# Performance work log

Hardware: AMD Instinct MI355X
Metric: run time of the kernel (lower is better)

The kernel has to match this reference:

```python
import jax, jax.numpy as jnp
import numpy as np

N_STEPS = 8          # spatial_interval
SPATIAL_SCALE = 1.0  # spatial_scale


def setup_inputs() -> dict:
    key = jax.random.key(0)
    ks = jax.random.split(key, 6)
    B, N, D = 32, 1024, 256
    x = jax.random.normal(ks[0], (B, N, D), dtype=jnp.float32)
    adj_mx = jax.random.uniform(ks[1], (N, N), dtype=jnp.float32) / N  # row-scaled dense adjacency
    alpha_train = jnp.ones((N,), dtype=jnp.float32)          # alpha * ones(num_node), alpha=1.0
    w = jnp.eye(D, dtype=jnp.float32) + 0.01 * jax.random.normal(ks[2], (D, D), dtype=jnp.float32)
    d = jax.random.uniform(ks[3], (D,), dtype=jnp.float32)
    fc_in_w = jax.random.normal(ks[4], (D, D), dtype=jnp.float32) * (1.0 / np.sqrt(D))
    fc_in_b = jnp.zeros((D,), dtype=jnp.float32)
    return {"x": x, "adj_mx": adj_mx, "alpha_train": alpha_train, "w": w,
            "d": d, "fc_in_w": fc_in_w, "fc_in_b": fc_in_b, "vt": 0}


def reference(x, adj_mx, alpha_train, w, d, fc_in_w, fc_in_b, vt):
    # x: [B, N, D]. x0 is detached in torch (x.clone().detach()).
    x0 = jax.lax.stop_gradient(x)
    # fc_in (dropout is identity in eval mode)
    h = jnp.einsum('bnd,ed->bne', x, fc_in_w) + fc_in_b
    # constants of the diffusion ODE
    alph = jax.nn.sigmoid(alpha_train)[:, None]          # [N, 1]
    d_clamped = jnp.clip(d, 0.0, 1.0)
    w_eff = (w * d_clamped) @ w.T                        # [D, D]
    dt = jnp.float32(SPATIAL_SCALE / N_STEPS)

    def euler_step(h, _):
        ax = jnp.einsum('nm,bmd->bnd', adj_mx, h)        # graph diffusion
        f = alph * 0.5 * (ax - h) + h @ w_eff - h + x0
        return h + dt * f, None

    h, _ = jax.lax.scan(euler_step, h, None, length=N_STEPS)
    return h
```

## Files before the change

### kernel.cpp

```cpp
#include <hip/hip_runtime.h>
#include <hip/hip_bf16.h>
#include <stdint.h>

typedef __bf16 bf16;
typedef __bf16 bf16x8 __attribute__((ext_vector_type(8)));
typedef __bf16 bf16x4 __attribute__((ext_vector_type(4)));
typedef float f32x4 __attribute__((ext_vector_type(4)));
typedef unsigned short u16;

__device__ __forceinline__ void gload_lds16(const bf16* g, bf16* l) {
    __builtin_amdgcn_global_load_lds(
        (const __attribute__((address_space(1))) void*)g,
        (__attribute__((address_space(3))) void*)l, 16, 0, 0);
}

__device__ __forceinline__ void stChunk(const bf16* __restrict__ g, int ld,
                                        bf16* l, int c) {
    int row = c >> 3, slot = c & 7;
    gload_lds16(g + (size_t)row * ld + ((slot ^ (row & 7)) << 3), l + c * 8);
}

__device__ __forceinline__ void mma8(const bf16x8& a0, const bf16x8& a1,
                                     const bf16x8& b0, const bf16x8& b1,
                                     const bf16x8& b2, const bf16x8& b3,
                                     f32x4 (&acc)[4][4], int mi) {
    acc[mi][0] = __builtin_amdgcn_mfma_f32_16x16x32_bf16(a0, b0, acc[mi][0], 0, 0, 0);
    acc[mi][1] = __builtin_amdgcn_mfma_f32_16x16x32_bf16(a0, b1, acc[mi][1], 0, 0, 0);
    acc[mi][2] = __builtin_amdgcn_mfma_f32_16x16x32_bf16(a0, b2, acc[mi][2], 0, 0, 0);
    acc[mi][3] = __builtin_amdgcn_mfma_f32_16x16x32_bf16(a0, b3, acc[mi][3], 0, 0, 0);
    acc[mi+1][0] = __builtin_amdgcn_mfma_f32_16x16x32_bf16(a1, b0, acc[mi+1][0], 0, 0, 0);
    acc[mi+1][1] = __builtin_amdgcn_mfma_f32_16x16x32_bf16(a1, b1, acc[mi+1][1], 0, 0, 0);
    acc[mi+1][2] = __builtin_amdgcn_mfma_f32_16x16x32_bf16(a1, b2, acc[mi+1][2], 0, 0, 0);
    acc[mi+1][3] = __builtin_amdgcn_mfma_f32_16x16x32_bf16(a1, b3, acc[mi+1][3], 0, 0, 0);
}

#define PHASE_SYNC_PRE()                                        \
    __builtin_amdgcn_s_barrier();                               \
    asm volatile("s_waitcnt lgkmcnt(0)" ::: "memory");          \
    __builtin_amdgcn_sched_barrier(0);                          \
    __builtin_amdgcn_s_setprio(1);
#define PHASE_SYNC_POST()                                       \
    __builtin_amdgcn_s_setprio(0);                              \
    __builtin_amdgcn_s_barrier();

__global__ void prep_alpha(const float* __restrict__ a, float* __restrict__ out) {
    int i = blockIdx.x * blockDim.x + threadIdx.x;
    if (i < 1024) out[i] = 0.5f / (1.0f + __expf(-a[i]));
}

__global__ void prep_adj(const float* __restrict__ adj, const float* __restrict__ ahs,
                         bf16* __restrict__ adjb) {
    int i = blockIdx.x * blockDim.x + threadIdx.x;
    int row = i >> 8;
    float s = ahs[row];
    float4 v = ((const float4*)adj)[i];
    bf16x4 o = {(bf16)(s * v.x), (bf16)(s * v.y), (bf16)(s * v.z), (bf16)(s * v.w)};
    ((bf16x4*)adjb)[i] = o;
}

__global__ void cast_f32_bf16x4(const float* __restrict__ src, bf16* __restrict__ dst,
                                int n4) {
    int i = blockIdx.x * blockDim.x + threadIdx.x;
    if (i < n4) {
        float4 v = ((const float4*)src)[i];
        bf16x4 o = {(bf16)v.x, (bf16)v.y, (bf16)v.z, (bf16)v.w};
        ((bf16x4*)dst)[i] = o;
    }
}

__global__ void prep_weff(const float* __restrict__ w, const float* __restrict__ dv,
                          bf16* __restrict__ weffT) {
    __shared__ float wk[256];
    __shared__ float dd[256];
    int k = blockIdx.x, j = threadIdx.x;
    dd[j] = fminf(fmaxf(dv[j], 0.0f), 1.0f);
    wk[j] = w[k * 256 + j];
    __syncthreads();
    float s = 0.0f;
#pragma unroll 8
    for (int c = 0; c < 256; ++c) s += wk[c] * dd[c] * w[j * 256 + c];
    weffT[j * 256 + k] = (bf16)s;
}

__global__ void prep_xT(const float* __restrict__ x, bf16* __restrict__ xT,
                        bf16* __restrict__ xb) {
    __shared__ bf16 tile[64][65];
    int b = blockIdx.z, n0 = blockIdx.x * 64, d0 = blockIdx.y * 64;
    int t = threadIdx.x;
    int i = t >> 4, j4 = (t & 15) * 4;
#pragma unroll
    for (int p = 0; p < 4; ++p) {
        int n = i + p * 16;
        size_t gi = (((size_t)b << 10) + n0 + n) * 256 + d0 + j4;
        float4 v = *(const float4*)&x[gi];
        bf16x4 o = {(bf16)v.x, (bf16)v.y, (bf16)v.z, (bf16)v.w};
        *(bf16x4*)&xb[gi] = o;
        tile[n][j4 + 0] = o[0]; tile[n][j4 + 1] = o[1];
        tile[n][j4 + 2] = o[2]; tile[n][j4 + 3] = o[3];
    }
    __syncthreads();
#pragma unroll
    for (int p = 0; p < 4; ++p) {
        int c = p * 256 + t;
        int d = c >> 4, nc = c & 15;
        bf16x4 o = {tile[nc * 4 + 0][d], tile[nc * 4 + 1][d],
                    tile[nc * 4 + 2][d], tile[nc * 4 + 3][d]};
        *(bf16x4*)&xT[(((size_t)(b * 256 + d0 + d)) << 10) + n0 + nc * 4] = o;
    }
}

__device__ __forceinline__ void stageA(const bf16* __restrict__ g, int lda,
                                       bf16* l, int t) {
#pragma unroll
    for (int i = 0; i < 4; ++i) stChunk(g, lda, l, (i << 8) + t);
}
__device__ __forceinline__ void stageB(const bf16* __restrict__ g, int ldb,
                                       bf16* l, int t) {
#pragma unroll
    for (int i = 0; i < 2; ++i) stChunk(g, ldb, l, (i << 8) + t);
}

__device__ __forceinline__ void mma_tile(const bf16* A, const bf16* B,
                                         f32x4 acc[2][4], int lane, int wv) {
    const int r0 = wv * 32 + (lane & 15);
    const int kq = lane >> 4;
    bf16x8 a[2][2], b[4][2];
#pragma unroll
    for (int mi = 0; mi < 2; ++mi) {
        int rA = r0 + mi * 16;
#pragma unroll
        for (int kk = 0; kk < 2; ++kk) {
            int kc = kk * 4 + kq;
            a[mi][kk] = *(const bf16x8*)&A[rA * 64 + ((kc ^ (rA & 7)) << 3)];
        }
    }
#pragma unroll
    for (int ni = 0; ni < 4; ++ni) {
        int rB = ni * 16 + (lane & 15);
#pragma unroll
        for (int kk = 0; kk < 2; ++kk) {
            int kc = kk * 4 + kq;
            b[ni][kk] = *(const bf16x8*)&B[rB * 64 + ((kc ^ (rB & 7)) << 3)];
        }
    }
#pragma unroll
    for (int kk = 0; kk < 2; ++kk)
#pragma unroll
        for (int mi = 0; mi < 2; ++mi)
#pragma unroll
            for (int ni = 0; ni < 4; ++ni)
                acc[mi][ni] = __builtin_amdgcn_mfma_f32_16x16x32_bf16(
                    a[mi][kk], b[ni][kk], acc[mi][ni], 0, 0, 0);
}

template <int NT, typename F>
__device__ __forceinline__ void run_pipeline(F tadr, bf16 (*As)[8192],
                                             bf16 (*Bs)[4096], f32x4 acc[2][4],
                                             int t, int lane, int wv) {
    {
        const bf16 *Ag, *Bg; int lda, ldb;
        tadr(0, Ag, lda, Bg, ldb);
        stageA(Ag, lda, As[0], t);
        stageB(Bg, ldb, Bs[0], t);
        if (NT > 1) {
            tadr(1, Ag, lda, Bg, ldb);
            stageA(Ag, lda, As[1], t);
            stageB(Bg, ldb, Bs[1], t);
        }
    }
    int cur = 0, pre = 2;
#pragma unroll 1
    for (int i = 0; i < NT; ++i) {
        if (i + 2 < NT) {
            const bf16 *Ag, *Bg; int lda, ldb;
            tadr(i + 2, Ag, lda, Bg, ldb);
            stageA(Ag, lda, As[pre], t);
            stageB(Bg, ldb, Bs[pre], t);
            asm volatile("s_waitcnt vmcnt(12)" ::: "memory");
        } else if (i + 1 < NT) {
            asm volatile("s_waitcnt vmcnt(6)" ::: "memory");
        } else {
            asm volatile("s_waitcnt vmcnt(0)" ::: "memory");
        }
        __builtin_amdgcn_s_barrier();
        __builtin_amdgcn_s_setprio(1);
        mma_tile(As[cur], Bs[cur], acc, lane, wv);
        __builtin_amdgcn_s_setprio(0);
        __builtin_amdgcn_s_barrier();
        cur = (cur == 2) ? 0 : cur + 1;
        pre = (pre == 2) ? 0 : pre + 1;
    }
}

__launch_bounds__(256, 2)
__global__ void gemm_fcin(const bf16* __restrict__ xb, const bf16* __restrict__ fcwb,
                          const float* __restrict__ fcb,
                          bf16* __restrict__ hb, bf16* __restrict__ hT,
                          bf16* __restrict__ hloT) {
    __shared__ __align__(16) bf16 As[3][8192];
    __shared__ __align__(16) bf16 Bs[3][4096];
    int t = threadIdx.x, lane = t & 63, wv = t >> 6;
    int row0 = blockIdx.y * 128;
    int col0 = blockIdx.x * 64;
    f32x4 acc[2][4] = {};
    const bf16* Ab = xb + (size_t)row0 * 256;
    const bf16* Bb = fcwb + (size_t)col0 * 256;
    auto tadr = [&](int i, const bf16*& Ag, int& lda, const bf16*& Bg, int& ldb) {
        Ag = Ab + i * 64; lda = 256;
        Bg = Bb + i * 64; ldb = 256;
    };
    run_pipeline<4>(tadr, As, Bs, acc, t, lane, wv);

    int rbase = row0 + wv * 32 + ((lane >> 4) << 2);
    int cbase = col0 + (lane & 15);
#pragma unroll
    for (int mi = 0; mi < 2; ++mi) {
        int rg = rbase + mi * 16;
#pragma unroll
        for (int ni = 0; ni < 4; ++ni) {
            int col = cbase + ni * 16;
            float bias = fcb[col];
            bf16x4 tv, lv;
#pragma unroll
            for (int r = 0; r < 4; ++r) {
                float v = acc[mi][ni][r] + bias;
                size_t idx = (size_t)(rg + r) * 256 + col;
                bf16 hi = (bf16)v;
                hb[idx] = hi;
                tv[r] = hi;
                lv[r] = (bf16)(v - (float)hi);
            }
            int b = rg >> 10, n = rg & 1023;
            size_t tb = (((size_t)(b * 256 + col)) << 10) + n;
            *(bf16x4*)&hT[tb] = tv;
            *(bf16x4*)&hloT[tb] = lv;
        }
    }
}

template <bool LAST>
__launch_bounds__(512, 1)
__global__ void gemm_step(const bf16* __restrict__ adjb, const bf16* __restrict__ hbp,
                          const bf16* __restrict__ hTp, const bf16* __restrict__ weffT,
                          const float* __restrict__ ahs, const bf16* __restrict__ xT,
                          bf16* __restrict__ hloT, bf16* __restrict__ hbn,
                          bf16* __restrict__ hTn, float* __restrict__ out) {
    __shared__ __align__(16) char smem[147456];
    bf16 (*As)[16384] = (bf16(*)[16384])smem;
    bf16 (*Bs)[8192]  = (bf16(*)[8192])(smem + 98304);
    int t = threadIdx.x, lane = t & 63, wv = t >> 6;
    int wm = wv >> 1, wn = wv & 1;
    int g = blockIdx.x;
    int xcd = g & 7, bidx = g >> 3;
    int b = (bidx & 3) * 8 + xcd;
    int tile = bidx >> 2;
    int n0 = (tile & 3) * 256;
    int d0 = (tile >> 2) * 128;
    f32x4 acc[4][4] = {};

    const bf16* A1 = adjb + (size_t)n0 * 1024;
    const bf16* B1 = hTp + ((size_t)(b * 256 + d0)) * 1024;
    const bf16* A2 = hbp + ((size_t)(b * 1024 + n0)) * 256;
    const bf16* B2 = weffT + (size_t)d0 * 256;
    auto tadr = [&](int i, const bf16*& Ag, int& la, const bf16*& Bg, int& lb) {
        if (i < 16) { Ag = A1 + i * 64; la = 1024; Bg = B1 + i * 64; lb = 1024; }
        else        { Ag = A2 + (i - 16) * 64; la = 256; Bg = B2 + (i - 16) * 64; lb = 256; }
    };
    const int NT = 20;
    {
        const bf16 *Ag, *Bg; int la, lb;
        tadr(0, Ag, la, Bg, lb);
#pragma unroll
        for (int k = 0; k < 4; ++k) stChunk(Ag, la, As[0], k * 512 + t);
#pragma unroll
        for (int k = 0; k < 2; ++k) stChunk(Bg, lb, Bs[0], k * 512 + t);
        tadr(1, Ag, la, Bg, lb);
#pragma unroll
        for (int k = 0; k < 4; ++k) stChunk(Ag, la, As[1], k * 512 + t);
#pragma unroll
        for (int k = 0; k < 2; ++k) stChunk(Bg, lb, Bs[1], k * 512 + t);
    }
    asm volatile("s_waitcnt vmcnt(6)" ::: "memory");
    __builtin_amdgcn_s_barrier();

    const int l15 = lane & 15, kq = lane >> 4;
    const int rA0 = wm * 64 + l15, rB0 = wn * 64 + l15;
    int cur = 0;
#pragma unroll 1
    for (int i = 0; i < NT; ++i) {
        const bf16* A = As[cur];
        const bf16* B = Bs[cur];
        int pre = cur + 2; if (pre >= 3) pre -= 3;
        const bf16 *Ag = nullptr, *Bg = nullptr; int la = 0, lb = 0;
        const bool st = (i + 2 < NT);
        if (st) tadr(i + 2, Ag, la, Bg, lb);

        bf16x8 a0, a1, b0, b1, b2, b3;
        {
            int kc = kq;
            b0 = *(const bf16x8*)&B[(rB0     ) * 64 + ((kc ^ ((rB0     ) & 7)) << 3)];
            b1 = *(const bf16x8*)&B[(rB0 + 16) * 64 + ((kc ^ ((rB0 + 16) & 7)) << 3)];
            b2 = *(const bf16x8*)&B[(rB0 + 32) * 64 + ((kc ^ ((rB0 + 32) & 7)) << 3)];
            b3 = *(const bf16x8*)&B[(rB0 + 48) * 64 + ((kc ^ ((rB0 + 48) & 7)) << 3)];
            a0 = *(const bf16x8*)&A[(rA0     ) * 64 + ((kc ^ ((rA0     ) & 7)) << 3)];
            a1 = *(const bf16x8*)&A[(rA0 + 16) * 64 + ((kc ^ ((rA0 + 16) & 7)) << 3)];
            if (st) { stChunk(Ag, la, As[pre], t); stChunk(Ag, la, As[pre], 512 + t); }
            PHASE_SYNC_PRE(); mma8(a0, a1, b0, b1, b2, b3, acc, 0); PHASE_SYNC_POST();
        }
        {
            int kc = kq;
            a0 = *(const bf16x8*)&A[(rA0 + 32) * 64 + ((kc ^ ((rA0 + 32) & 7)) << 3)];
            a1 = *(const bf16x8*)&A[(rA0 + 48) * 64 + ((kc ^ ((rA0 + 48) & 7)) << 3)];
            if (st) { stChunk(Ag, la, As[pre], 1024 + t); stChunk(Ag, la, As[pre], 1536 + t); }
            PHASE_SYNC_PRE(); mma8(a0, a1, b0, b1, b2, b3, acc, 2); PHASE_SYNC_POST();
        }
        {
            int kc = 4 + kq;
            b0 = *(const bf16x8*)&B[(rB0     ) * 64 + ((kc ^ ((rB0     ) & 7)) << 3)];
            b1 = *(const bf16x8*)&B[(rB0 + 16) * 64 + ((kc ^ ((rB0 + 16) & 7)) << 3)];
            b2 = *(const bf16x8*)&B[(rB0 + 32) * 64 + ((kc ^ ((rB0 + 32) & 7)) << 3)];
            b3 = *(const bf16x8*)&B[(rB0 + 48) * 64 + ((kc ^ ((rB0 + 48) & 7)) << 3)];
            a0 = *(const bf16x8*)&A[(rA0     ) * 64 + ((kc ^ ((rA0     ) & 7)) << 3)];
            a1 = *(const bf16x8*)&A[(rA0 + 16) * 64 + ((kc ^ ((rA0 + 16) & 7)) << 3)];
            if (st) { stChunk(Bg, lb, Bs[pre], t); stChunk(Bg, lb, Bs[pre], 512 + t); }
            PHASE_SYNC_PRE(); mma8(a0, a1, b0, b1, b2, b3, acc, 0); PHASE_SYNC_POST();
        }
        {
            int kc = 4 + kq;
            a0 = *(const bf16x8*)&A[(rA0 + 32) * 64 + ((kc ^ ((rA0 + 32) & 7)) << 3)];
            a1 = *(const bf16x8*)&A[(rA0 + 48) * 64 + ((kc ^ ((rA0 + 48) & 7)) << 3)];
            if (st) asm volatile("s_waitcnt vmcnt(6)" ::: "memory");
            else    asm volatile("s_waitcnt vmcnt(0)" ::: "memory");
            PHASE_SYNC_PRE(); mma8(a0, a1, b0, b1, b2, b3, acc, 2); PHASE_SYNC_POST();
        }
        cur = cur + 1; if (cur == 3) cur = 0;
    }

    const float dt = 0.125f;
    const int lq = (lane >> 4) << 2;
    bf16* img = (bf16*)smem;
    const int PADN = 260;
#pragma unroll
    for (int mi = 0; mi < 4; ++mi) {
        int nl = wm * 64 + mi * 16 + lq;
        int ng = n0 + nl;
        f32x4 av = *(const f32x4*)&ahs[ng];
#pragma unroll
        for (int ni = 0; ni < 4; ++ni) {
            int cl = wn * 64 + ni * 16 + l15;
            int cg = d0 + cl;
            size_t tb = (((size_t)(b * 256 + cg)) << 10) + ng;
            bf16x4 hp = *(const bf16x4*)&hTp[tb];
            bf16x4 lp = *(const bf16x4*)&hloT[tb];
            bf16x4 xp = *(const bf16x4*)&xT[tb];
            bf16x4 nhi, nlo;
#pragma unroll
            for (int r = 0; r < 4; ++r) {
                float hold = (float)hp[r] + (float)lp[r];
                float f = acc[mi][ni][r] - (av[r] + 1.0f) * hold + (float)xp[r];
                float hv = hold + dt * f;
                if (LAST) {
                    out[(((size_t)b << 10) + ng + r) * 256 + cg] = hv;
                } else {
                    bf16 hi2 = (bf16)hv;
                    nhi[r] = hi2;
                    nlo[r] = (bf16)(hv - (float)hi2);
                }
            }
            if (!LAST) {
                *(bf16x4*)&hTn[tb] = nhi;
                *(bf16x4*)&hloT[tb] = nlo;
                int nsw = nl ^ (((cl >> 3) & 7) << 2);
                *(bf16x4*)&img[cl * PADN + nsw] = nhi;
            }
        }
    }
    if (!LAST) {
        asm volatile("s_waitcnt lgkmcnt(0)" ::: "memory");
        __builtin_amdgcn_s_barrier();
        const u16* imgu = (const u16*)img;
#pragma unroll
        for (int P = 0; P < 8; ++P) {
            int chunk = P * 512 + t;
            int node = chunk >> 4;
            int c8 = chunk & 15;
            u16 v[8];
#pragma unroll
            for (int k = 0; k < 8; ++k) {
                int col = c8 * 8 + k;
                v[k] = imgu[col * PADN + (node ^ (((col >> 3) & 7) << 2))];
            }
            uint4 pk;
            pk.x = v[0] | ((unsigned)v[1] << 16);
            pk.y = v[2] | ((unsigned)v[3] << 16);
            pk.z = v[4] | ((unsigned)v[5] << 16);
            pk.w = v[6] | ((unsigned)v[7] << 16);
            *(uint4*)&hbn[(((size_t)b << 10) + n0 + node) * 256 + d0 + c8 * 8] = pk;
        }
    }
}

extern "C" void kernel_launch(void* const* d_in, const int* in_sizes, int n_in,
                              void* d_out, int out_size, void* d_ws, size_t ws_size,
                              hipStream_t stream) {
    const float* x     = (const float*)d_in[0];
    const float* adj   = (const float*)d_in[1];
    const float* alpha = (const float*)d_in[2];
    const float* w     = (const float*)d_in[3];
    const float* dvec  = (const float*)d_in[4];
    const float* fcw   = (const float*)d_in[5];
    const float* fcb   = (const float*)d_in[6];
    float* out = (float*)d_out;

    const size_t HB = (size_t)32 * 1024 * 256 * 2;
    char* p = (char*)d_ws;
    bf16* hb0   = (bf16*)p; p += HB;
    bf16* hb1   = (bf16*)p; p += HB;
    bf16* hT0   = (bf16*)p; p += HB;
    bf16* hT1   = (bf16*)p; p += HB;
    bf16* xb    = (bf16*)p; p += HB;
    bf16* hloT  = (bf16*)p; p += HB;
    bf16* xT    = (bf16*)p; p += HB;
    bf16* adjb  = (bf16*)p; p += (size_t)1024 * 1024 * 2;
    bf16* fcwb  = (bf16*)p; p += 256 * 256 * 2;
    bf16* weffT = (bf16*)p; p += 256 * 256 * 2;
    float* ahs  = (float*)p; p += 1024 * 4;

    prep_alpha<<<4, 256, 0, stream>>>(alpha, ahs);
    prep_adj<<<1024, 256, 0, stream>>>(adj, ahs, adjb);
    prep_weff<<<256, 256, 0, stream>>>(w, dvec, weffT);
    prep_xT<<<dim3(16, 4, 32), 256, 0, stream>>>(x, xT, xb);
    cast_f32_bf16x4<<<64, 256, 0, stream>>>(fcw, fcwb, 16384);

    gemm_fcin<<<dim3(4, 256), 256, 0, stream>>>(xb, fcwb, fcb, hb0, hT0, hloT);

    bf16* hb[2] = {hb0, hb1};
    bf16* hT[2] = {hT0, hT1};
    int cur = 0;
    for (int s = 0; s < 8; ++s) {
        if (s < 7)
            gemm_step<false><<<256, 512, 0, stream>>>(
                adjb, hb[cur], hT[cur], weffT, ahs, xT, hloT,
                hb[cur ^ 1], hT[cur ^ 1], out);
        else
            gemm_step<true><<<256, 512, 0, stream>>>(
                adjb, hb[cur], hT[cur], weffT, ahs, xT, hloT,
                hb[cur ^ 1], hT[cur ^ 1], out);
        cur ^= 1;
    }
}
```

Measured before the change: 404.9 us.

## Software-pipeline LDS fragment loads across k-halves in the diffusion step GEMM

```diff
diff --git a/kernel.cpp b/kernel.cpp
--- a/kernel.cpp
+++ b/kernel.cpp
@@ -20,28 +20,8 @@
     gload_lds16(g + (size_t)row * ld + ((slot ^ (row & 7)) << 3), l + c * 8);
 }
 
-__device__ __forceinline__ void mma8(const bf16x8& a0, const bf16x8& a1,
-                                     const bf16x8& b0, const bf16x8& b1,
-                                     const bf16x8& b2, const bf16x8& b3,
-                                     f32x4 (&acc)[4][4], int mi) {
-    acc[mi][0] = __builtin_amdgcn_mfma_f32_16x16x32_bf16(a0, b0, acc[mi][0], 0, 0, 0);
-    acc[mi][1] = __builtin_amdgcn_mfma_f32_16x16x32_bf16(a0, b1, acc[mi][1], 0, 0, 0);
-    acc[mi][2] = __builtin_amdgcn_mfma_f32_16x16x32_bf16(a0, b2, acc[mi][2], 0, 0, 0);
-    acc[mi][3] = __builtin_amdgcn_mfma_f32_16x16x32_bf16(a0, b3, acc[mi][3], 0, 0, 0);
-    acc[mi+1][0] = __builtin_amdgcn_mfma_f32_16x16x32_bf16(a1, b0, acc[mi+1][0], 0, 0, 0);
-    acc[mi+1][1] = __builtin_amdgcn_mfma_f32_16x16x32_bf16(a1, b1, acc[mi+1][1], 0, 0, 0);
-    acc[mi+1][2] = __builtin_amdgcn_mfma_f32_16x16x32_bf16(a1, b2, acc[mi+1][2], 0, 0, 0);
-    acc[mi+1][3] = __builtin_amdgcn_mfma_f32_16x16x32_bf16(a1, b3, acc[mi+1][3], 0, 0, 0);
-}
-
-#define PHASE_SYNC_PRE()                                        \
-    __builtin_amdgcn_s_barrier();                               \
-    asm volatile("s_waitcnt lgkmcnt(0)" ::: "memory");          \
-    __builtin_amdgcn_sched_barrier(0);                          \
-    __builtin_amdgcn_s_setprio(1);
-#define PHASE_SYNC_POST()                                       \
-    __builtin_amdgcn_s_setprio(0);                              \
-    __builtin_amdgcn_s_barrier();
+#define LDSW(buf, row, kc) \
+    (*(const bf16x8*)&(buf)[(row) * 64 + ((((kc) ^ ((row) & 7))) << 3)])
 
 __global__ void prep_alpha(const float* __restrict__ a, float* __restrict__ out) {
     int i = blockIdx.x * blockDim.x + threadIdx.x;
@@ -109,13 +89,13 @@
     }
 }
 
-__device__ __forceinline__ void stageA(const bf16* __restrict__ g, int lda,
-                                       bf16* l, int t) {
+__device__ __forceinline__ void stageA4(const bf16* __restrict__ g, int lda,
+                                        bf16* l, int t) {
 #pragma unroll
     for (int i = 0; i < 4; ++i) stChunk(g, lda, l, (i << 8) + t);
 }
-__device__ __forceinline__ void stageB(const bf16* __restrict__ g, int ldb,
-                                       bf16* l, int t) {
+__device__ __forceinline__ void stageB2(const bf16* __restrict__ g, int ldb,
+                                        bf16* l, int t) {
 #pragma unroll
     for (int i = 0; i < 2; ++i) stChunk(g, ldb, l, (i << 8) + t);
 }
@@ -129,19 +109,13 @@
     for (int mi = 0; mi < 2; ++mi) {
         int rA = r0 + mi * 16;
 #pragma unroll
-        for (int kk = 0; kk < 2; ++kk) {
-            int kc = kk * 4 + kq;
-            a[mi][kk] = *(const bf16x8*)&A[rA * 64 + ((kc ^ (rA & 7)) << 3)];
-        }
+        for (int kk = 0; kk < 2; ++kk) a[mi][kk] = LDSW(A, rA, kk * 4 + kq);
     }
 #pragma unroll
     for (int ni = 0; ni < 4; ++ni) {
         int rB = ni * 16 + (lane & 15);
 #pragma unroll
-        for (int kk = 0; kk < 2; ++kk) {
-            int kc = kk * 4 + kq;
-            b[ni][kk] = *(const bf16x8*)&B[rB * 64 + ((kc ^ (rB & 7)) << 3)];
-        }
+        for (int kk = 0; kk < 2; ++kk) b[ni][kk] = LDSW(B, rB, kk * 4 + kq);
     }
 #pragma unroll
     for (int kk = 0; kk < 2; ++kk)
@@ -160,12 +134,12 @@
     {
         const bf16 *Ag, *Bg; int lda, ldb;
         tadr(0, Ag, lda, Bg, ldb);
-        stageA(Ag, lda, As[0], t);
-        stageB(Bg, ldb, Bs[0], t);
+        stageA4(Ag, lda, As[0], t);
+        stageB2(Bg, ldb, Bs[0], t);
         if (NT > 1) {
             tadr(1, Ag, lda, Bg, ldb);
-            stageA(Ag, lda, As[1], t);
-            stageB(Bg, ldb, Bs[1], t);
+            stageA4(Ag, lda, As[1], t);
+            stageB2(Bg, ldb, Bs[1], t);
         }
     }
     int cur = 0, pre = 2;
@@ -174,8 +148,8 @@
         if (i + 2 < NT) {
             const bf16 *Ag, *Bg; int lda, ldb;
             tadr(i + 2, Ag, lda, Bg, ldb);
-            stageA(Ag, lda, As[pre], t);
-            stageB(Bg, ldb, Bs[pre], t);
+            stageA4(Ag, lda, As[pre], t);
+            stageB2(Bg, ldb, Bs[pre], t);
             asm volatile("s_waitcnt vmcnt(12)" ::: "memory");
         } else if (i + 1 < NT) {
             asm volatile("s_waitcnt vmcnt(6)" ::: "memory");
@@ -280,60 +254,83 @@
 #pragma unroll
         for (int k = 0; k < 2; ++k) stChunk(Bg, lb, Bs[1], k * 512 + t);
     }
+    const int l15 = lane & 15, kq = lane >> 4;
+    const int rA[4] = {wm * 64 + l15, wm * 64 + 16 + l15,
+                       wm * 64 + 32 + l15, wm * 64 + 48 + l15};
+    const int rB[4] = {wn * 64 + l15, wn * 64 + 16 + l15,
+                       wn * 64 + 32 + l15, wn * 64 + 48 + l15};
+
     asm volatile("s_waitcnt vmcnt(6)" ::: "memory");
     __builtin_amdgcn_s_barrier();
 
-    const int l15 = lane & 15, kq = lane >> 4;
-    const int rA0 = wm * 64 + l15, rB0 = wn * 64 + l15;
+    bf16x8 pa[4], pb[4];
+#pragma unroll
+    for (int j = 0; j < 4; ++j) pb[j] = LDSW(Bs[0], rB[j], kq);
+#pragma unroll
+    for (int j = 0; j < 4; ++j) pa[j] = LDSW(As[0], rA[j], kq);
+
     int cur = 0;
 #pragma unroll 1
     for (int i = 0; i < NT; ++i) {
-        const bf16* A = As[cur];
-        const bf16* B = Bs[cur];
+        const bf16* Ab = As[cur];
+        const bf16* Bb = Bs[cur];
+        int nxt = cur + 1; if (nxt == 3) nxt = 0;
         int pre = cur + 2; if (pre >= 3) pre -= 3;
+        const bool st2 = (i + 2 < NT), st1 = (i + 1 < NT);
         const bf16 *Ag = nullptr, *Bg = nullptr; int la = 0, lb = 0;
-        const bool st = (i + 2 < NT);
-        if (st) tadr(i + 2, Ag, la, Bg, lb);
-
-        bf16x8 a0, a1, b0, b1, b2, b3;
-        {
-            int kc = kq;
-            b0 = *(const bf16x8*)&B[(rB0     ) * 64 + ((kc ^ ((rB0     ) & 7)) << 3)];
-            b1 = *(const bf16x8*)&B[(rB0 + 16) * 64 + ((kc ^ ((rB0 + 16) & 7)) << 3)];
-            b2 = *(const bf16x8*)&B[(rB0 + 32) * 64 + ((kc ^ ((rB0 + 32) & 7)) << 3)];
-            b3 = *(const bf16x8*)&B[(rB0 + 48) * 64 + ((kc ^ ((rB0 + 48) & 7)) << 3)];
-            a0 = *(const bf16x8*)&A[(rA0     ) * 64 + ((kc ^ ((rA0     ) & 7)) << 3)];
-            a1 = *(const bf16x8*)&A[(rA0 + 16) * 64 + ((kc ^ ((rA0 + 16) & 7)) << 3)];
-            if (st) { stChunk(Ag, la, As[pre], t); stChunk(Ag, la, As[pre], 512 + t); }
-            PHASE_SYNC_PRE(); mma8(a0, a1, b0, b1, b2, b3, acc, 0); PHASE_SYNC_POST();
-        }
-        {
-            int kc = kq;
-            a0 = *(const bf16x8*)&A[(rA0 + 32) * 64 + ((kc ^ ((rA0 + 32) & 7)) << 3)];
-            a1 = *(const bf16x8*)&A[(rA0 + 48) * 64 + ((kc ^ ((rA0 + 48) & 7)) << 3)];
-            if (st) { stChunk(Ag, la, As[pre], 1024 + t); stChunk(Ag, la, As[pre], 1536 + t); }
-            PHASE_SYNC_PRE(); mma8(a0, a1, b0, b1, b2, b3, acc, 2); PHASE_SYNC_POST();
-        }
-        {
-            int kc = 4 + kq;
-            b0 = *(const bf16x8*)&B[(rB0     ) * 64 + ((kc ^ ((rB0     ) & 7)) << 3)];
-            b1 = *(const bf16x8*)&B[(rB0 + 16) * 64 + ((kc ^ ((rB0 + 16) & 7)) << 3)];
-            b2 = *(const bf16x8*)&B[(rB0 + 32) * 64 + ((kc ^ ((rB0 + 32) & 7)) << 3)];
-            b3 = *(const bf16x8*)&B[(rB0 + 48) * 64 + ((kc ^ ((rB0 + 48) & 7)) << 3)];
-            a0 = *(const bf16x8*)&A[(rA0     ) * 64 + ((kc ^ ((rA0     ) & 7)) << 3)];
-            a1 = *(const bf16x8*)&A[(rA0 + 16) * 64 + ((kc ^ ((rA0 + 16) & 7)) << 3)];
-            if (st) { stChunk(Bg, lb, Bs[pre], t); stChunk(Bg, lb, Bs[pre], 512 + t); }
-            PHASE_SYNC_PRE(); mma8(a0, a1, b0, b1, b2, b3, acc, 0); PHASE_SYNC_POST();
-        }
-        {
-            int kc = 4 + kq;
-            a0 = *(const bf16x8*)&A[(rA0 + 32) * 64 + ((kc ^ ((rA0 + 32) & 7)) << 3)];
-            a1 = *(const bf16x8*)&A[(rA0 + 48) * 64 + ((kc ^ ((rA0 + 48) & 7)) << 3)];
-            if (st) asm volatile("s_waitcnt vmcnt(6)" ::: "memory");
-            else    asm volatile("s_waitcnt vmcnt(0)" ::: "memory");
-            PHASE_SYNC_PRE(); mma8(a0, a1, b0, b1, b2, b3, acc, 2); PHASE_SYNC_POST();
-        }
-        cur = cur + 1; if (cur == 3) cur = 0;
+        if (st2) tadr(i + 2, Ag, la, Bg, lb);
+
+        bf16x8 qa[4], qb[4];
+#pragma unroll
+        for (int j = 0; j < 4; ++j) qb[j] = LDSW(Bb, rB[j], 4 + kq);
+#pragma unroll
+        for (int j = 0; j < 4; ++j) qa[j] = LDSW(Ab, rA[j], 4 + kq);
+        if (st2) {
+            stChunk(Ag, la, As[pre], t);        stChunk(Ag, la, As[pre], 512 + t);
+            stChunk(Ag, la, As[pre], 1024 + t); stChunk(Ag, la, As[pre], 1536 + t);
+        }
+        __builtin_amdgcn_s_barrier();
+        asm volatile("s_waitcnt lgkmcnt(8)" ::: "memory");
+        __builtin_amdgcn_sched_barrier(0);
+        __builtin_amdgcn_s_setprio(1);
+#pragma unroll
+        for (int mi = 0; mi < 4; ++mi)
+#pragma unroll
+            for (int ni = 0; ni < 4; ++ni)
+                acc[mi][ni] = __builtin_amdgcn_mfma_f32_16x16x32_bf16(
+                    pa[mi], pb[ni], acc[mi][ni], 0, 0, 0);
+        __builtin_amdgcn_s_setprio(0);
+        __builtin_amdgcn_s_barrier();
+
+        if (st2) {
+            stChunk(Bg, lb, Bs[pre], t); stChunk(Bg, lb, Bs[pre], 512 + t);
+            asm volatile("s_waitcnt vmcnt(6)" ::: "memory");
+        } else {
+            asm volatile("s_waitcnt vmcnt(0)" ::: "memory");
+        }
+        __builtin_amdgcn_s_barrier();
+        if (st1) {
+            const bf16* An = As[nxt];
+            const bf16* Bn = Bs[nxt];
+#pragma unroll
+            for (int j = 0; j < 4; ++j) pb[j] = LDSW(Bn, rB[j], kq);
+#pragma unroll
+            for (int j = 0; j < 4; ++j) pa[j] = LDSW(An, rA[j], kq);
+            asm volatile("s_waitcnt lgkmcnt(8)" ::: "memory");
+        } else {
+            asm volatile("s_waitcnt lgkmcnt(0)" ::: "memory");
+        }
+        __builtin_amdgcn_sched_barrier(0);
+        __builtin_amdgcn_s_setprio(1);
+#pragma unroll
+        for (int mi = 0; mi < 4; ++mi)
+#pragma unroll
+            for (int ni = 0; ni < 4; ++ni)
+                acc[mi][ni] = __builtin_amdgcn_mfma_f32_16x16x32_bf16(
+                    qa[mi], qb[ni], acc[mi][ni], 0, 0, 0);
+        __builtin_amdgcn_s_setprio(0);
+        __builtin_amdgcn_s_barrier();
+        cur = nxt;
     }
 
     const float dt = 0.125f;
```

New measurement: 397.3 us. No clear change (-1.9%).
